# Kernel tuning notes

Measured on AMD Instinct MI355X. Metric: run time of the kernel, lower is better.

The kernel has to match this reference:

```python
import jax, jax.numpy as jnp
import numpy as np

B, D = 8192, 1024
C, K = 1000, 8
EPS = 1e-15


def setup_inputs() -> dict:
    key = jax.random.key(0)
    k1, k2 = jax.random.split(key)
    # points inside the unit Poincare ball (c=1): scale so E||x|| ~ 0.64 < 1
    x = jax.random.normal(k1, (B, D), dtype=jnp.float32) * 0.02
    weight_v = jax.random.normal(k2, (C, K, D), dtype=jnp.float32)
    weight_g = jnp.ones((C,), dtype=jnp.float32)
    gamma = jnp.ones((), dtype=jnp.float32)
    return {"x": x, "weight_v": weight_v, "weight_g": weight_g, "gamma": gamma}


def reference(x, weight_v, weight_g, gamma):
    # PoincareBall curvature c = 1.0 -> rc = sqrt(c) = 1.0
    rc = jnp.asarray(1.0, dtype=x.dtype)
    # unit prototype directions: [C, K, D]
    z_norm = jnp.maximum(jnp.linalg.norm(weight_v, axis=-1, keepdims=True), EPS)
    z_unit = weight_v / z_norm
    rcx = rc * x                                   # [B, D]
    cx2 = jnp.sum(rcx * rcx, axis=-1, keepdims=True)  # [B, 1]
    inner = jnp.einsum('bd,ckd->bck', rcx, z_unit)    # [B, C, K]
    drcr = 2.0 * rc * gamma
    num = 2.0 * inner * jnp.cosh(drcr) - (1.0 + cx2[:, :, None]) * jnp.sinh(drcr)
    den = jnp.maximum(1.0 - cx2, EPS)              # [B, 1]
    logits_ck = (2.0 * weight_g[None, :, None] / rc) * jnp.arcsinh(num / den[:, :, None])
    logits = jax.nn.logsumexp(logits_ck, axis=-1)  # [B, C]
    return logits
```

## Files before the change

kernel.cpp:

```cpp
#include <hip/hip_runtime.h>
#include <hip/hip_bf16.h>
#include <stdint.h>

#define B_ROWS 8192
#define D_DIM  1024
#define C_CLS  1000
#define K_PROT 8
#define N_PAD  8192
#define BKT    64
#define NT     16

typedef __attribute__((ext_vector_type(8))) short  short8;
typedef __attribute__((ext_vector_type(4))) float  f32x4;


__device__ __forceinline__ ushort f2bf(float f) {
    union { float f; uint32_t u; } v; v.f = f;
    uint32_t u = v.u;
    return (ushort)((u + 0x7fffu + ((u >> 16) & 1u)) >> 16);
}

typedef __attribute__((address_space(1))) void gv_t;
typedef __attribute__((address_space(3))) void lv_t;

__device__ __forceinline__ void gload_lds16(const void* g, void* l) {
    __builtin_amdgcn_global_load_lds((gv_t*)g, (lv_t*)l, 16, 0, 0);
}

__device__ __forceinline__ float waveReduceSum(float s) {
    #pragma unroll
    for (int m = 32; m >= 1; m >>= 1) s += __shfl_xor(s, m);
    return s;
}


__global__ __launch_bounds__(256) void prep_z(const float* __restrict__ wv,
                                              ushort* __restrict__ zb) {
    const int P = blockIdx.x;
    const int t = threadIdx.x;
    __shared__ float red[4];

    const int gpan = P >> 6;
    const int ni   = (P >> 4) & 3;
    const int cc   = P & 15;
    const int cls  = gpan * 8 + (cc & 7);
    const int k    = ni + ((cc >> 3) << 2);

    if (cls >= C_CLS) {
        ((ushort4*)(zb + (size_t)P * D_DIM))[t] = make_ushort4(0, 0, 0, 0);
        return;
    }
    const int n = cls * K_PROT + k;
    const float4 v = ((const float4*)(wv + (size_t)n * D_DIM))[t];
    float s = v.x*v.x + v.y*v.y + v.z*v.z + v.w*v.w;
    s = waveReduceSum(s);
    if ((t & 63) == 0) red[t >> 6] = s;
    __syncthreads();
    const float n2 = red[0] + red[1] + red[2] + red[3];
    const float rn = 1.0f / fmaxf(sqrtf(n2), 1e-15f);
    ushort4 o;
    o.x = f2bf(v.x * rn); o.y = f2bf(v.y * rn);
    o.z = f2bf(v.z * rn); o.w = f2bf(v.w * rn);
    ((ushort4*)(zb + (size_t)P * D_DIM))[t] = o;
}


__global__ __launch_bounds__(256) void prep_x(const float* __restrict__ x,
                                              ushort* __restrict__ xb,
                                              float* __restrict__ cx2) {
    const int b = blockIdx.x;
    const int t = threadIdx.x;
    __shared__ float red[4];

    const float4 v = ((const float4*)(x + (size_t)b * D_DIM))[t];
    ushort4 o;
    o.x = f2bf(v.x); o.y = f2bf(v.y); o.z = f2bf(v.z); o.w = f2bf(v.w);
    ((ushort4*)(xb + (size_t)b * D_DIM))[t] = o;

    float s = v.x*v.x + v.y*v.y + v.z*v.z + v.w*v.w;
    s = waveReduceSum(s);
    if ((t & 63) == 0) red[t >> 6] = s;
    __syncthreads();
    if (t == 0) cx2[b] = red[0] + red[1] + red[2] + red[3];
}


__global__ __launch_bounds__(512, 2) void gemm_epi(
        const ushort* __restrict__ A,
        const ushort* __restrict__ Bz,
        const float*  __restrict__ cx2g,
        const float*  __restrict__ wgl,
        const float*  __restrict__ gamma_p,
        float*        __restrict__ out)
{
    __shared__ __attribute__((aligned(128))) char lds[131072];

    const int tid  = threadIdx.x;
    const int lane = tid & 63;
    const int wid  = tid >> 6;
    const int wm   = wid >> 2;
    const int wn   = wid & 3;

    const int bid = blockIdx.x;
    const int xcd = bid & 7;
    const int j   = bid >> 3;
    const int bn  = xcd * 4 + (j & 3);
    const int bm  = j >> 2;
    const int m0  = bm * 256;
    const int n0  = bn * 256;

    const int aCol = (((tid & 3) ^ ((tid >> 2) & 3)) * 8);
    const ushort* aP = A  + (size_t)(m0 + (tid >> 2)) * D_DIM + aCol;
    const ushort* bP = Bz + (size_t)(n0 + (tid >> 2)) * D_DIM + aCol;
    const int ldsW = wid * 1024;

    const int swz   = (((lane >> 4) ^ (lane & 3)) * 16);
    const int aRowB = (wm * 128 + (lane & 15)) * 64 + swz;
    const int bRowB = (wn * 64  + (lane & 15)) * 64 + swz;

#define BUF(c)  (lds + ((c) & 1) * 65536)
#define STAGE_A(c, h) do { char* d_ = BUF(c) + (h) * 16384 + ldsW; \
    const ushort* s_ = aP + (c) * BKT + (h) * 32; \
    gload_lds16(s_, d_); \
    gload_lds16(s_ + (size_t)128 * D_DIM, d_ + 8192); } while (0)
#define STAGE_B(c, h) do { char* d_ = BUF(c) + 32768 + (h) * 16384 + ldsW; \
    const ushort* s_ = bP + (c) * BKT + (h) * 32; \
    gload_lds16(s_, d_); \
    gload_lds16(s_ + (size_t)128 * D_DIM, d_ + 8192); } while (0)
#define LDA(c, h, mi) (*(const short8*)(BUF(c) + (h) * 16384 + aRowB + (mi) * 1024))
#define LDB(c, h, ni) (*(const short8*)(BUF(c) + 32768 + (h) * 16384 + bRowB + (ni) * 1024))
#define BAR() do { asm volatile("" ::: "memory"); \
    __builtin_amdgcn_s_barrier(); asm volatile("" ::: "memory"); } while (0)

    f32x4 acc[8][4];
    #pragma unroll
    for (int i = 0; i < 8; ++i)
        #pragma unroll
        for (int q = 0; q < 4; ++q) acc[i][q] = (f32x4)(0.0f);

    STAGE_A(0, 0); STAGE_B(0, 0); STAGE_A(0, 1); STAGE_B(0, 1);
    STAGE_A(1, 0); STAGE_B(1, 0);
    asm volatile("s_waitcnt vmcnt(4)" ::: "memory");
    BAR();

    for (int c = 0; c < NT; ++c) {
        short8 a[4], b[4];
        #pragma unroll
        for (int mi = 0; mi < 4; ++mi) a[mi] = LDA(c, 0, mi);
        #pragma unroll
        for (int ni = 0; ni < 4; ++ni) b[ni] = LDB(c, 0, ni);
        if (c + 1 < NT) STAGE_A(c + 1, 1);
        BAR();
        __builtin_amdgcn_s_setprio(1);
        #pragma unroll
        for (int mi = 0; mi < 4; ++mi)
            #pragma unroll
            for (int ni = 0; ni < 4; ++ni)
                acc[mi][ni] = __builtin_amdgcn_mfma_f32_16x16x32_bf16(
                    a[mi], b[ni], acc[mi][ni], 0, 0, 0);
        __builtin_amdgcn_s_setprio(0);
        BAR();
        #pragma unroll
        for (int mi = 0; mi < 4; ++mi) a[mi] = LDA(c, 0, mi + 4);
        if (c + 1 < NT) STAGE_B(c + 1, 1);
        BAR();
        __builtin_amdgcn_s_setprio(1);
        #pragma unroll
        for (int mi = 0; mi < 4; ++mi)
            #pragma unroll
            for (int ni = 0; ni < 4; ++ni)
                acc[mi + 4][ni] = __builtin_amdgcn_mfma_f32_16x16x32_bf16(
                    a[mi], b[ni], acc[mi + 4][ni], 0, 0, 0);
        __builtin_amdgcn_s_setprio(0);
        BAR();
        #pragma unroll
        for (int mi = 0; mi < 4; ++mi) a[mi] = LDA(c, 1, mi);
        #pragma unroll
        for (int ni = 0; ni < 4; ++ni) b[ni] = LDB(c, 1, ni);
        if (c + 2 < NT) STAGE_A(c + 2, 0);
        BAR();
        __builtin_amdgcn_s_setprio(1);
        #pragma unroll
        for (int mi = 0; mi < 4; ++mi)
            #pragma unroll
            for (int ni = 0; ni < 4; ++ni)
                acc[mi][ni] = __builtin_amdgcn_mfma_f32_16x16x32_bf16(
                    a[mi], b[ni], acc[mi][ni], 0, 0, 0);
        __builtin_amdgcn_s_setprio(0);
        BAR();
        #pragma unroll
        for (int mi = 0; mi < 4; ++mi) a[mi] = LDA(c, 1, mi + 4);
        if (c + 2 < NT) STAGE_B(c + 2, 0);
        BAR();
        __builtin_amdgcn_s_setprio(1);
        #pragma unroll
        for (int mi = 0; mi < 4; ++mi)
            #pragma unroll
            for (int ni = 0; ni < 4; ++ni)
                acc[mi + 4][ni] = __builtin_amdgcn_mfma_f32_16x16x32_bf16(
                    a[mi], b[ni], acc[mi + 4][ni], 0, 0, 0);
        __builtin_amdgcn_s_setprio(0);
        if (c < NT - 2)       asm volatile("s_waitcnt vmcnt(4)" ::: "memory");
        else if (c == NT - 2) asm volatile("s_waitcnt vmcnt(0)" ::: "memory");
        BAR();
    }

    __syncthreads();
    float* scx = (float*)lds;
    if (tid < 256) scx[tid] = cx2g[m0 + tid];
    __syncthreads();

    const float gam = gamma_p[0];
    const float ex  = expf(2.0f * gam);
    const float ch2 = ex + 1.0f / ex;
    const float sh  = 0.5f * (ex - 1.0f / ex);

    const int  pan = (n0 >> 6) + wn;
    const int  cls = pan * 8 + (lane & 7);
    const bool wrt = ((lane & 8) == 0) && (cls < C_CLS);
    const float w2 = (cls < C_CLS) ? 2.0f * wgl[cls] : 0.0f;

    #pragma unroll
    for (int mi = 0; mi < 8; ++mi) {
        #pragma unroll
        for (int r = 0; r < 4; ++r) {
            const int mloc = wm * 128 + mi * 16 + ((lane >> 4) << 2) + r;
            const float c2   = scx[mloc];
            const float rden = 1.0f / fmaxf(1.0f - c2, 1e-15f);
            const float tc   = ch2 * rden;
            const float tp   = (1.0f + c2) * sh * rden;
            float bk[4];
            #pragma unroll
            for (int ni = 0; ni < 4; ++ni) {
                const float t = fmaf(acc[mi][ni][r], tc, -tp);
                const float u = fmaxf(t + __fsqrt_rn(fmaf(t, t, 1.0f)), 1e-20f);
                bk[ni] = w2 * __logf(u);
            }
            float mx = fmaxf(fmaxf(bk[0], bk[1]), fmaxf(bk[2], bk[3]));
            mx = fmaxf(mx, __shfl_xor(mx, 8));
            float s = __expf(bk[0] - mx) + __expf(bk[1] - mx)
                    + __expf(bk[2] - mx) + __expf(bk[3] - mx);
            s += __shfl_xor(s, 8);
            if (wrt)
                out[(size_t)(m0 + mloc) * C_CLS + cls] = mx + __logf(s);
        }
    }
#undef BUF
#undef STAGE_A
#undef STAGE_B
#undef LDA
#undef LDB
#undef BAR
}


extern "C" void kernel_launch(void* const* d_in, const int* in_sizes, int n_in,
                              void* d_out, int out_size, void* d_ws, size_t ws_size,
                              hipStream_t stream) {
    const float* x     = (const float*)d_in[0];
    const float* wv    = (const float*)d_in[1];
    const float* wg    = (const float*)d_in[2];
    const float* gamma = (const float*)d_in[3];
    float* out = (float*)d_out;

    char* ws = (char*)d_ws;
    ushort* xb  = (ushort*)ws;
    ushort* zb  = (ushort*)(ws + (size_t)B_ROWS * D_DIM * 2);
    float*  cx2 = (float*)(ws + (size_t)B_ROWS * D_DIM * 2
                              + (size_t)N_PAD * D_DIM * 2);

    prep_z<<<N_PAD, 256, 0, stream>>>(wv, zb);
    prep_x<<<B_ROWS, 256, 0, stream>>>(x, xb, cx2);
    gemm_epi<<<1024, 512, 0, stream>>>(xb, zb, cx2, wg, gamma, out);
}
```

Before: 206.5 us.

## Merge prep kernels and restructure GEMM LDS staging to full-K tiles with fewer barriers

Fuses the two preprocessing kernels into a single launch that handles both x rows and prototype rows, with a new prototype-row permutation matching the GEMM's B layout. The GEMM main loop now stages a whole 64-wide K tile per buffer with 128-byte rows and an XOR swizzle over 8 chunks. The loop is reorganised into quadrant sub-steps (A halves x B halves) with one prefetch of the next tile and one barrier per sub-step, removing the extra barriers between phases. This is meant to cut launch overhead and synchronisation stalls, at the cost of a tighter single-tile-ahead prefetch depth and a more intricate waitcnt schedule.

```diff
diff --git a/kernel.cpp b/kernel.cpp
--- a/kernel.cpp
+++ b/kernel.cpp
@@ -34,17 +34,33 @@
 }
 
 
-__global__ __launch_bounds__(256) void prep_z(const float* __restrict__ wv,
-                                              ushort* __restrict__ zb) {
-    const int P = blockIdx.x;
+__global__ __launch_bounds__(256) void prep(const float* __restrict__ x,
+                                            const float* __restrict__ wv,
+                                            ushort* __restrict__ xb,
+                                            ushort* __restrict__ zb,
+                                            float* __restrict__ cx2) {
     const int t = threadIdx.x;
     __shared__ float red[4];
 
-    const int gpan = P >> 6;
-    const int ni   = (P >> 4) & 3;
-    const int cc   = P & 15;
-    const int cls  = gpan * 8 + (cc & 7);
-    const int k    = ni + ((cc >> 3) << 2);
+    if ((int)blockIdx.x < B_ROWS) {
+        const int b = blockIdx.x;
+        const float4 v = ((const float4*)(x + (size_t)b * D_DIM))[t];
+        ushort4 o;
+        o.x = f2bf(v.x); o.y = f2bf(v.y); o.z = f2bf(v.z); o.w = f2bf(v.w);
+        ((ushort4*)(xb + (size_t)b * D_DIM))[t] = o;
+        float s = v.x*v.x + v.y*v.y + v.z*v.z + v.w*v.w;
+        s = waveReduceSum(s);
+        if ((t & 63) == 0) red[t >> 6] = s;
+        __syncthreads();
+        if (t == 0) cx2[b] = red[0] + red[1] + red[2] + red[3];
+        return;
+    }
+
+    const int P   = blockIdx.x - B_ROWS;
+    const int pan = (P >> 8) * 4 + ((P >> 5) & 3);
+    const int ni  = 2 * ((P >> 7) & 1) + ((P >> 4) & 1);
+    const int cls = pan * 8 + (P & 7);
+    const int k   = ni + 4 * ((P >> 3) & 1);
 
     if (cls >= C_CLS) {
         ((ushort4*)(zb + (size_t)P * D_DIM))[t] = make_ushort4(0, 0, 0, 0);
@@ -65,26 +81,6 @@
 }
 
 
-__global__ __launch_bounds__(256) void prep_x(const float* __restrict__ x,
-                                              ushort* __restrict__ xb,
-                                              float* __restrict__ cx2) {
-    const int b = blockIdx.x;
-    const int t = threadIdx.x;
-    __shared__ float red[4];
-
-    const float4 v = ((const float4*)(x + (size_t)b * D_DIM))[t];
-    ushort4 o;
-    o.x = f2bf(v.x); o.y = f2bf(v.y); o.z = f2bf(v.z); o.w = f2bf(v.w);
-    ((ushort4*)(xb + (size_t)b * D_DIM))[t] = o;
-
-    float s = v.x*v.x + v.y*v.y + v.z*v.z + v.w*v.w;
-    s = waveReduceSum(s);
-    if ((t & 63) == 0) red[t >> 6] = s;
-    __syncthreads();
-    if (t == 0) cx2[b] = red[0] + red[1] + red[2] + red[3];
-}
-
-
 __global__ __launch_bounds__(512, 2) void gemm_epi(
         const ushort* __restrict__ A,
         const ushort* __restrict__ Bz,
@@ -109,27 +105,29 @@
     const int m0  = bm * 256;
     const int n0  = bn * 256;
 
-    const int aCol = (((tid & 3) ^ ((tid >> 2) & 3)) * 8);
-    const ushort* aP = A  + (size_t)(m0 + (tid >> 2)) * D_DIM + aCol;
-    const ushort* bP = Bz + (size_t)(n0 + (tid >> 2)) * D_DIM + aCol;
+    const int stCol = ((tid & 7) ^ ((tid >> 3) & 7)) * 8;
+    const int stRow = tid >> 3;
+    const ushort* aSrc0 = A  + (size_t)(m0 + stRow) * D_DIM + stCol;
+    const ushort* bSrc0 = Bz + (size_t)(n0 + stRow) * D_DIM + stCol;
     const int ldsW = wid * 1024;
 
-    const int swz   = (((lane >> 4) ^ (lane & 3)) * 16);
-    const int aRowB = (wm * 128 + (lane & 15)) * 64 + swz;
-    const int bRowB = (wn * 64  + (lane & 15)) * 64 + swz;
-
-#define BUF(c)  (lds + ((c) & 1) * 65536)
-#define STAGE_A(c, h) do { char* d_ = BUF(c) + (h) * 16384 + ldsW; \
-    const ushort* s_ = aP + (c) * BKT + (h) * 32; \
-    gload_lds16(s_, d_); \
-    gload_lds16(s_ + (size_t)128 * D_DIM, d_ + 8192); } while (0)
-#define STAGE_B(c, h) do { char* d_ = BUF(c) + 32768 + (h) * 16384 + ldsW; \
-    const ushort* s_ = bP + (c) * BKT + (h) * 32; \
-    gload_lds16(s_, d_); \
-    gload_lds16(s_ + (size_t)128 * D_DIM, d_ + 8192); } while (0)
-#define LDA(c, h, mi) (*(const short8*)(BUF(c) + (h) * 16384 + aRowB + (mi) * 1024))
-#define LDB(c, h, ni) (*(const short8*)(BUF(c) + 32768 + (h) * 16384 + bRowB + (ni) * 1024))
-#define BAR() do { asm volatile("" ::: "memory"); \
+    const int swz0 = ((      (lane >> 4) * 16) ^ ((lane & 7) << 4));
+    const int swz1 = ((64 + ((lane >> 4) * 16)) ^ ((lane & 7) << 4));
+    const int aBase = (wm * 64 + (lane & 15)) * 128;
+    const int bBase = 32768 + (wn * 32 + (lane & 15)) * 128;
+
+#define ABYTE(mi) (aBase + ((mi) >> 2) * 16384 + ((mi) & 3) * 2048)
+#define BBYTE(ni) (bBase + ((ni) >> 1) * 16384 + ((ni) & 1) * 2048)
+#define STG_A(buf, ct, i, roff) \
+    gload_lds16(aSrc0 + (size_t)(roff) * D_DIM + (ct) * BKT, (buf) + (i) * 8192 + ldsW)
+#define STG_B(buf, ct, i) \
+    gload_lds16(bSrc0 + (size_t)(i) * 64 * D_DIM + (ct) * BKT, (buf) + 32768 + (i) * 8192 + ldsW)
+#define STAGE_AE(buf, ct) do { STG_A(buf, ct, 0, 0);  STG_A(buf, ct, 1, 128); } while (0)
+#define STAGE_AO(buf, ct) do { STG_A(buf, ct, 2, 64); STG_A(buf, ct, 3, 192); } while (0)
+#define STAGE_BE(buf, ct) do { STG_B(buf, ct, 0); STG_B(buf, ct, 1); } while (0)
+#define STAGE_BO(buf, ct) do { STG_B(buf, ct, 2); STG_B(buf, ct, 3); } while (0)
+#define VMC(n) asm volatile("s_waitcnt vmcnt(" #n ")" ::: "memory")
+#define BAR()  do { asm volatile("" ::: "memory"); \
     __builtin_amdgcn_s_barrier(); asm volatile("" ::: "memory"); } while (0)
 
     f32x4 acc[8][4];
@@ -138,71 +136,104 @@
         #pragma unroll
         for (int q = 0; q < 4; ++q) acc[i][q] = (f32x4)(0.0f);
 
-    STAGE_A(0, 0); STAGE_B(0, 0); STAGE_A(0, 1); STAGE_B(0, 1);
-    STAGE_A(1, 0); STAGE_B(1, 0);
-    asm volatile("s_waitcnt vmcnt(4)" ::: "memory");
+    {
+        char* b0 = lds;
+        STAGE_AE(b0, 0); STAGE_BE(b0, 0); STAGE_AO(b0, 0); STAGE_BO(b0, 0);
+    }
+    VMC(4);
     BAR();
 
     for (int c = 0; c < NT; ++c) {
-        short8 a[4], b[4];
-        #pragma unroll
-        for (int mi = 0; mi < 4; ++mi) a[mi] = LDA(c, 0, mi);
-        #pragma unroll
-        for (int ni = 0; ni < 4; ++ni) b[ni] = LDB(c, 0, ni);
-        if (c + 1 < NT) STAGE_A(c + 1, 1);
+        const char* cur = lds + (c & 1) * 65536;
+        char*       nxt = lds + ((c + 1) & 1) * 65536;
+        const bool  st  = (c + 1 < NT);
+        short8 a[4][2], b[2][2];
+
+        #pragma unroll
+        for (int mi = 0; mi < 4; ++mi) {
+            a[mi][0] = *(const short8*)(cur + ABYTE(mi) + swz0);
+            a[mi][1] = *(const short8*)(cur + ABYTE(mi) + swz1);
+        }
+        #pragma unroll
+        for (int ni = 0; ni < 2; ++ni) {
+            b[ni][0] = *(const short8*)(cur + BBYTE(ni) + swz0);
+            b[ni][1] = *(const short8*)(cur + BBYTE(ni) + swz1);
+        }
+        if (st) { STAGE_AE(nxt, c + 1); VMC(4); } else { VMC(2); }
         BAR();
         __builtin_amdgcn_s_setprio(1);
         #pragma unroll
         for (int mi = 0; mi < 4; ++mi)
             #pragma unroll
-            for (int ni = 0; ni < 4; ++ni)
+            for (int ni = 0; ni < 2; ++ni) {
                 acc[mi][ni] = __builtin_amdgcn_mfma_f32_16x16x32_bf16(
-                    a[mi], b[ni], acc[mi][ni], 0, 0, 0);
+                    a[mi][0], b[ni][0], acc[mi][ni], 0, 0, 0);
+                acc[mi][ni] = __builtin_amdgcn_mfma_f32_16x16x32_bf16(
+                    a[mi][1], b[ni][1], acc[mi][ni], 0, 0, 0);
+            }
         __builtin_amdgcn_s_setprio(0);
-        BAR();
-        #pragma unroll
-        for (int mi = 0; mi < 4; ++mi) a[mi] = LDA(c, 0, mi + 4);
-        if (c + 1 < NT) STAGE_B(c + 1, 1);
+
+        #pragma unroll
+        for (int mi = 0; mi < 4; ++mi) {
+            a[mi][0] = *(const short8*)(cur + ABYTE(mi + 4) + swz0);
+            a[mi][1] = *(const short8*)(cur + ABYTE(mi + 4) + swz1);
+        }
+        if (st) { STAGE_BE(nxt, c + 1); VMC(4); } else { VMC(0); }
         BAR();
         __builtin_amdgcn_s_setprio(1);
         #pragma unroll
         for (int mi = 0; mi < 4; ++mi)
             #pragma unroll
-            for (int ni = 0; ni < 4; ++ni)
+            for (int ni = 0; ni < 2; ++ni) {
                 acc[mi + 4][ni] = __builtin_amdgcn_mfma_f32_16x16x32_bf16(
-                    a[mi], b[ni], acc[mi + 4][ni], 0, 0, 0);
+                    a[mi][0], b[ni][0], acc[mi + 4][ni], 0, 0, 0);
+                acc[mi + 4][ni] = __builtin_amdgcn_mfma_f32_16x16x32_bf16(
+                    a[mi][1], b[ni][1], acc[mi + 4][ni], 0, 0, 0);
+            }
         __builtin_amdgcn_s_setprio(0);
-        BAR();
-        #pragma unroll
-        for (int mi = 0; mi < 4; ++mi) a[mi] = LDA(c, 1, mi);
-        #pragma unroll
-        for (int ni = 0; ni < 4; ++ni) b[ni] = LDB(c, 1, ni);
-        if (c + 2 < NT) STAGE_A(c + 2, 0);
+
+        #pragma unroll
+        for (int mi = 0; mi < 4; ++mi) {
+            a[mi][0] = *(const short8*)(cur + ABYTE(mi) + swz0);
+            a[mi][1] = *(const short8*)(cur + ABYTE(mi) + swz1);
+        }
+        #pragma unroll
+        for (int ni = 0; ni < 2; ++ni) {
+            b[ni][0] = *(const short8*)(cur + BBYTE(ni + 2) + swz0);
+            b[ni][1] = *(const short8*)(cur + BBYTE(ni + 2) + swz1);
+        }
+        if (st) STAGE_AO(nxt, c + 1);
         BAR();
         __builtin_amdgcn_s_setprio(1);
         #pragma unroll
         for (int mi = 0; mi < 4; ++mi)
             #pragma unroll
-            for (int ni = 0; ni < 4; ++ni)
-                acc[mi][ni] = __builtin_amdgcn_mfma_f32_16x16x32_bf16(
-                    a[mi], b[ni], acc[mi][ni], 0, 0, 0);
+            for (int ni = 0; ni < 2; ++ni) {
+                acc[mi][ni + 2] = __builtin_amdgcn_mfma_f32_16x16x32_bf16(
+                    a[mi][0], b[ni][0], acc[mi][ni + 2], 0, 0, 0);
+                acc[mi][ni + 2] = __builtin_amdgcn_mfma_f32_16x16x32_bf16(
+                    a[mi][1], b[ni][1], acc[mi][ni + 2], 0, 0, 0);
+            }
         __builtin_amdgcn_s_setprio(0);
-        BAR();
-        #pragma unroll
-        for (int mi = 0; mi < 4; ++mi) a[mi] = LDA(c, 1, mi + 4);
-        if (c + 2 < NT) STAGE_B(c + 2, 0);
+
+        #pragma unroll
+        for (int mi = 0; mi < 4; ++mi) {
+            a[mi][0] = *(const short8*)(cur + ABYTE(mi + 4) + swz0);
+            a[mi][1] = *(const short8*)(cur + ABYTE(mi + 4) + swz1);
+        }
+        if (st) { STAGE_BO(nxt, c + 1); VMC(4); }
         BAR();
         __builtin_amdgcn_s_setprio(1);
         #pragma unroll
         for (int mi = 0; mi < 4; ++mi)
             #pragma unroll
-            for (int ni = 0; ni < 4; ++ni)
-                acc[mi + 4][ni] = __builtin_amdgcn_mfma_f32_16x16x32_bf16(
-                    a[mi], b[ni], acc[mi + 4][ni], 0, 0, 0);
+            for (int ni = 0; ni < 2; ++ni) {
+                acc[mi + 4][ni + 2] = __builtin_amdgcn_mfma_f32_16x16x32_bf16(
+                    a[mi][0], b[ni][0], acc[mi + 4][ni + 2], 0, 0, 0);
+                acc[mi + 4][ni + 2] = __builtin_amdgcn_mfma_f32_16x16x32_bf16(
+                    a[mi][1], b[ni][1], acc[mi + 4][ni + 2], 0, 0, 0);
+            }
         __builtin_amdgcn_s_setprio(0);
-        if (c < NT - 2)       asm volatile("s_waitcnt vmcnt(4)" ::: "memory");
-        else if (c == NT - 2) asm volatile("s_waitcnt vmcnt(0)" ::: "memory");
-        BAR();
     }
 
     __syncthreads();
@@ -215,7 +246,7 @@
     const float ch2 = ex + 1.0f / ex;
     const float sh  = 0.5f * (ex - 1.0f / ex);
 
-    const int  pan = (n0 >> 6) + wn;
+    const int  pan = bn * 4 + wn;
     const int  cls = pan * 8 + (lane & 7);
     const bool wrt = ((lane & 8) == 0) && (cls < C_CLS);
     const float w2 = (cls < C_CLS) ? 2.0f * wgl[cls] : 0.0f;
@@ -245,11 +276,15 @@
                 out[(size_t)(m0 + mloc) * C_CLS + cls] = mx + __logf(s);
         }
     }
-#undef BUF
-#undef STAGE_A
-#undef STAGE_B
-#undef LDA
-#undef LDB
+#undef ABYTE
+#undef BBYTE
+#undef STG_A
+#undef STG_B
+#undef STAGE_AE
+#undef STAGE_AO
+#undef STAGE_BE
+#undef STAGE_BO
+#undef VMC
 #undef BAR
 }
 
@@ -269,7 +304,6 @@
     float*  cx2 = (float*)(ws + (size_t)B_ROWS * D_DIM * 2
                               + (size_t)N_PAD * D_DIM * 2);
 
-    prep_z<<<N_PAD, 256, 0, stream>>>(wv, zb);
-    prep_x<<<B_ROWS, 256, 0, stream>>>(x, xb, cx2);
+    prep<<<B_ROWS + N_PAD, 256, 0, stream>>>(x, wv, xb, zb, cx2);
     gemm_epi<<<1024, 512, 0, stream>>>(xb, zb, cx2, wg, gamma, out);
 }
```

Result: faster. 192.5 us (-6.8%).
